# Optimization experiments

Measured on AMD Instinct MI355X. Metric: run time of the kernel, lower is better.

The kernel has to match this reference:

```python
import jax, jax.numpy as jnp
import numpy as np

N1, N2, N3, N4, D = 50000, 100000, 200000, 300000, 256


def setup_inputs() -> dict:
    key = jax.random.key(0)
    ks = jax.random.split(key, 10)
    feat = jax.random.normal(ks[0], (N1, D), dtype=jnp.float32) * 0.5  # scaled so level-4 products stay bounded
    c2a = jax.random.randint(ks[1], (N2,), 0, N1)
    c2b = jax.random.randint(ks[2], (N2,), 0, N1)
    c3a = jax.random.randint(ks[3], (N3,), 0, N2)
    c3b = jax.random.randint(ks[4], (N3,), 0, N2)
    c4a = jax.random.randint(ks[5], (N4,), 0, N3)
    c4b = jax.random.randint(ks[6], (N4,), 0, N3)
    W = jax.random.normal(ks[7], (D, D), dtype=jnp.float32) / jnp.sqrt(jnp.float32(D))
    b = jax.random.normal(ks[8], (D,), dtype=jnp.float32) * 0.01
    return {"feat": feat, "c2a": c2a, "c2b": c2b, "c3a": c3a, "c3b": c3b,
            "c4a": c4a, "c4b": c4b, "W": W, "b": b}


def _scatter_sum(h_parent, ca, cb, num_children):
    # each parent sends its feature to both children; children sum incoming messages
    z = jnp.zeros((num_children, h_parent.shape[1]), dtype=h_parent.dtype)
    return z.at[ca].add(h_parent).at[cb].add(h_parent)


def reference(feat, c2a, c2b, c3a, c3b, c4a, c4b, W, b):
    # upward: prod reduction over the two constituent subpaths (mailbox prod, dim=1)
    h1 = feat
    h2 = h1[c2a] * h1[c2b]            # [N2, D]
    h3 = h2[c3a] * h2[c3b]            # [N3, D]
    h4 = h3[c4a] * h3[c4b]            # [N4, D]
    # downward: sum-scatter parent -> children, h = h + h_down
    h3 = h3 + _scatter_sum(h4, c4a, c4b, h3.shape[0])
    h2 = h2 + _scatter_sum(h3, c3a, c3b, h2.shape[0])
    h1 = h1 + _scatter_sum(h2, c2a, c2b, h1.shape[0])
    # apply_nodes on n1: Linear + SiLU
    out = jax.nn.silu(h1 @ W + b)
    return out
```

## Files before the change

kernel.cpp:

```cpp
#include <hip/hip_runtime.h>
#include <cstdint>
#include <cstddef>

#define DD 256
#define DH 128
#define SCAN_BLK 256
#define SCAN_ELEMS 2048

__device__ __forceinline__ float2 mul2(float2 a, float2 b) {
    return make_float2(a.x * b.x, a.y * b.y);
}
__device__ __forceinline__ float2 add2(float2 a, float2 b) {
    return make_float2(a.x + b.x, a.y + b.y);
}
__device__ __forceinline__ float2 ldh(const float* __restrict__ base, int row, int lane) {
    return ((const float2*)(base + (size_t)row * DH))[lane];
}
__device__ __forceinline__ float2 ldf(const float* __restrict__ base, int row, int doff, int lane) {
    return ((const float2*)(base + (size_t)row * DD + doff))[lane];
}

__global__ void k_count_pairs(const int* __restrict__ ea, const int* __restrict__ eb,
                              int ne, int* __restrict__ cnt) {
    int e = blockIdx.x * blockDim.x + threadIdx.x;
    if (e >= ne) return;
    atomicAdd(&cnt[ea[e]], 1);
    atomicAdd(&cnt[eb[e]], 1);
}

__global__ void k_fill_edges(const int* __restrict__ ea, const int* __restrict__ eb,
                             int ne, int* __restrict__ cursor, int* __restrict__ ent) {
    int e = blockIdx.x * blockDim.x + threadIdx.x;
    if (e >= ne) return;
    int a = ea[e], b = eb[e];
    int pa = atomicAdd(&cursor[a], 1);
    int pb = atomicAdd(&cursor[b], 1);
    ent[pa] = e;
    ent[pb] = e;
}

__global__ void k_fill_pairs4(const int* __restrict__ c4a, const int* __restrict__ c4b,
                              const int* __restrict__ c3a, const int* __restrict__ c3b,
                              int ne, int* __restrict__ cursor, int2* __restrict__ entp) {
    int e = blockIdx.x * blockDim.x + threadIdx.x;
    if (e >= ne) return;
    int a = c4a[e], b = c4b[e];
    int2 prA = make_int2(c3a[b], c3b[b]);
    int2 prB = make_int2(c3a[a], c3b[a]);
    int pa = atomicAdd(&cursor[a], 1);
    int pb = atomicAdd(&cursor[b], 1);
    entp[pa] = prA;
    entp[pb] = prB;
}

__global__ void k_block_sums(const int* __restrict__ cnt, int n, int* __restrict__ bsum) {
    __shared__ int sdata[SCAN_BLK];
    int base = blockIdx.x * SCAN_ELEMS;
    int s = 0;
#pragma unroll
    for (int k = 0; k < 8; ++k) {
        int idx = base + threadIdx.x + k * SCAN_BLK;
        if (idx < n) s += cnt[idx];
    }
    sdata[threadIdx.x] = s;
    __syncthreads();
    for (int off = SCAN_BLK / 2; off > 0; off >>= 1) {
        if (threadIdx.x < off) sdata[threadIdx.x] += sdata[threadIdx.x + off];
        __syncthreads();
    }
    if (threadIdx.x == 0) bsum[blockIdx.x] = sdata[0];
}

__global__ void k_scan_bsums(int* __restrict__ bsum, int nb, int* __restrict__ total_out) {
    if (threadIdx.x == 0 && blockIdx.x == 0) {
        int acc = 0;
        for (int b = 0; b < nb; ++b) { int v = bsum[b]; bsum[b] = acc; acc += v; }
        *total_out = acc;
    }
}

__global__ void k_scan_final(const int* __restrict__ cnt, int n,
                             const int* __restrict__ bsum, int* __restrict__ offs) {
    __shared__ int sdata[SCAN_BLK];
    int base = blockIdx.x * SCAN_ELEMS;
    int t0 = base + threadIdx.x * 8;
    int loc[8];
    int s = 0;
#pragma unroll
    for (int k = 0; k < 8; ++k) {
        int idx = t0 + k;
        int v = (idx < n) ? cnt[idx] : 0;
        loc[k] = s;
        s += v;
    }
    sdata[threadIdx.x] = s;
    __syncthreads();
    int run = s;
    for (int off = 1; off < SCAN_BLK; off <<= 1) {
        int add = (threadIdx.x >= (unsigned)off) ? sdata[threadIdx.x - off] : 0;
        __syncthreads();
        run += add;
        sdata[threadIdx.x] = run;
        __syncthreads();
    }
    int texcl = run - s + bsum[blockIdx.x];
#pragma unroll
    for (int k = 0; k < 8; ++k) {
        int idx = t0 + k;
        if (idx < n) offs[idx] = texcl + loc[k];
    }
}

__global__ void k_h2_half(const float* __restrict__ feat, const int* __restrict__ c2a,
                          const int* __restrict__ c2b, float* __restrict__ h2h,
                          int n2, int doff) {
    int q = blockIdx.x * 4 + (threadIdx.x >> 6);
    int lane = threadIdx.x & 63;
    if (q >= n2) return;
    float2 v = mul2(ldf(feat, c2a[q], doff, lane), ldf(feat, c2b[q], doff, lane));
    ((float2*)(h2h + (size_t)q * DH))[lane] = v;
}

__global__ void k_h3tot_half(const float* __restrict__ h2h,
                             const int* __restrict__ c3a, const int* __restrict__ c3b,
                             const int* __restrict__ offs4, const int2* __restrict__ entp,
                             float* __restrict__ h3th, int lo, int hi) {
    int j = lo + blockIdx.x * 4 + (threadIdx.x >> 6);
    int lane = threadIdx.x & 63;
    if (j >= hi) return;
    float2 own = mul2(ldh(h2h, c3a[j], lane), ldh(h2h, c3b[j], lane));
    float2 s = make_float2(0.f, 0.f);
    int e0 = offs4[j], e1 = offs4[j + 1];
    int e = e0;
    for (; e + 1 < e1; e += 2) {
        int2 p0 = entp[e], p1 = entp[e + 1];
        float2 a0 = ldh(h2h, p0.x, lane), b0 = ldh(h2h, p0.y, lane);
        float2 a1 = ldh(h2h, p1.x, lane), b1 = ldh(h2h, p1.y, lane);
        s = add2(s, add2(mul2(a0, b0), mul2(a1, b1)));
    }
    if (e < e1) {
        int2 p = entp[e];
        s = add2(s, mul2(ldh(h2h, p.x, lane), ldh(h2h, p.y, lane)));
    }
    float2 r = mul2(own, make_float2(1.f + s.x, 1.f + s.y));
    ((float2*)(h3th + (size_t)(j - lo) * DH))[lane] = r;
}

__global__ void k_m2_half(const float* __restrict__ h2h,
                          const int* __restrict__ offs3, const int* __restrict__ ent3,
                          const float* __restrict__ h3th, float* __restrict__ dst,
                          int n2, int lo, int hi, int first) {
    int q = blockIdx.x * 4 + (threadIdx.x >> 6);
    int lane = threadIdx.x & 63;
    if (q >= n2) return;
    float2 h = first ? ldh(h2h, q, lane) : ldh(dst, q, lane);
    int f0 = offs3[q], f1 = offs3[q + 1];
    int f = f0;
    for (; f + 1 < f1; f += 2) {
        int j0 = ent3[f], j1 = ent3[f + 1];
        bool in0 = (j0 >= lo) && (j0 < hi);
        bool in1 = (j1 >= lo) && (j1 < hi);
        if (in0 && in1) {
            h = add2(h, add2(ldh(h3th, j0 - lo, lane), ldh(h3th, j1 - lo, lane)));
        } else if (in0) {
            h = add2(h, ldh(h3th, j0 - lo, lane));
        } else if (in1) {
            h = add2(h, ldh(h3th, j1 - lo, lane));
        }
    }
    if (f < f1) {
        int j0 = ent3[f];
        if (j0 >= lo && j0 < hi) h = add2(h, ldh(h3th, j0 - lo, lane));
    }
    ((float2*)(dst + (size_t)q * DH))[lane] = h;
}

__global__ void k_h1_half(const float* __restrict__ feat, const float* __restrict__ m2,
                          const int* __restrict__ offs2, const int* __restrict__ ent2,
                          float* __restrict__ out, int n1, int doff) {
    int i = blockIdx.x * 4 + (threadIdx.x >> 6);
    int lane = threadIdx.x & 63;
    if (i >= n1) return;
    float2 h = ldf(feat, i, doff, lane);
    int e0 = offs2[i], e1 = offs2[i + 1];
    int e = e0;
    for (; e + 1 < e1; e += 2) {
        int q0 = ent2[e], q1 = ent2[e + 1];
        h = add2(h, add2(ldh(m2, q0, lane), ldh(m2, q1, lane)));
    }
    if (e < e1) h = add2(h, ldh(m2, ent2[e], lane));
    ((float2*)(out + (size_t)i * DD + doff))[lane] = h;
}

__device__ __forceinline__ float silu_f(float x) { return x / (1.0f + expf(-x)); }

__global__ __launch_bounds__(256) void k_gemm_silu(float* __restrict__ h,
                                                   const float* __restrict__ W,
                                                   const float* __restrict__ bias,
                                                   int n1) {
    __shared__ float As[32 * DD];
    const int t = threadIdx.x;
    const int row0 = blockIdx.x * 32;

    const float4* hv = (const float4*)h;
    float4* As4 = (float4*)As;
#pragma unroll
    for (int i = 0; i < 8; ++i) {
        int idx = t + i * 256;
        int r = idx >> 6, c = idx & 63;
        int gr = row0 + r;
        float4 v = make_float4(0.f, 0.f, 0.f, 0.f);
        if (gr < n1) v = hv[(size_t)gr * 64 + c];
        As4[idx] = v;
    }
    __syncthreads();

    const int rg = t >> 6;
    const int cg = t & 63;
    const float4* Wv = (const float4*)W;

    float4 acc[8];
#pragma unroll
    for (int r = 0; r < 8; ++r) acc[r] = make_float4(0.f, 0.f, 0.f, 0.f);

    for (int k = 0; k < DD; k += 4) {
        float4 a[8];
#pragma unroll
        for (int r = 0; r < 8; ++r)
            a[r] = *(const float4*)&As[(rg * 8 + r) * DD + k];
#pragma unroll
        for (int kk = 0; kk < 4; ++kk) {
            float4 w = Wv[(size_t)(k + kk) * 64 + cg];
#pragma unroll
            for (int r = 0; r < 8; ++r) {
                float av = (kk == 0) ? a[r].x : (kk == 1) ? a[r].y
                         : (kk == 2) ? a[r].z : a[r].w;
                acc[r].x += av * w.x;
                acc[r].y += av * w.y;
                acc[r].z += av * w.z;
                acc[r].w += av * w.w;
            }
        }
    }

    float4 bb = ((const float4*)bias)[cg];
    float4* ho = (float4*)h;
#pragma unroll
    for (int r = 0; r < 8; ++r) {
        int gr = row0 + rg * 8 + r;
        if (gr >= n1) continue;
        float4 x = acc[r];
        x.x = silu_f(x.x + bb.x);
        x.y = silu_f(x.y + bb.y);
        x.z = silu_f(x.z + bb.z);
        x.w = silu_f(x.w + bb.w);
        ho[(size_t)gr * 64 + cg] = x;
    }
}

static inline size_t al16(size_t x) { return (x + 15) & ~(size_t)15; }

extern "C" void kernel_launch(void* const* d_in, const int* in_sizes, int n_in,
                              void* d_out, int out_size, void* d_ws, size_t ws_size,
                              hipStream_t stream) {
    const float* feat = (const float*)d_in[0];
    const int* c2a = (const int*)d_in[1];
    const int* c2b = (const int*)d_in[2];
    const int* c3a = (const int*)d_in[3];
    const int* c3b = (const int*)d_in[4];
    const int* c4a = (const int*)d_in[5];
    const int* c4b = (const int*)d_in[6];
    const float* W = (const float*)d_in[7];
    const float* bias = (const float*)d_in[8];

    const int N1 = in_sizes[0] / DD;
    const int N2 = in_sizes[1];
    const int N3 = in_sizes[3];
    const int N4 = in_sizes[5];
    float* out = (float*)d_out;
    char* ws = (char*)d_ws;

    dim3 blk(256);
    auto rows_grid = [](int n) { return dim3((unsigned)((n + 3) / 4)); };
    auto thr_grid = [](int n) { return dim3((unsigned)((n + 255) / 256)); };

    int maxN = N1 > N2 ? N1 : N2;
    if (N3 > maxN) maxN = N3;

    size_t cnt_b   = al16((size_t)maxN * 4);
    size_t bsum_b  = al16(4096);
    size_t offs4_b = al16((size_t)(N3 + 1) * 4);
    size_t entp_b  = al16((size_t)2 * N4 * 8);
    size_t offs3_b = al16((size_t)(N2 + 1) * 4);
    size_t ent3_b  = al16((size_t)2 * N3 * 4);
    size_t offs2_b = al16((size_t)(N1 + 1) * 4);
    size_t ent2_b  = al16((size_t)2 * N2 * 4);
    size_t fixed_b = cnt_b + bsum_b + offs4_b + entp_b + offs3_b + ent3_b +
                     offs2_b + ent2_b;
    size_t h2h_b = (size_t)N2 * DH * sizeof(float);
    size_t h3th_full_b = (size_t)N3 * DH * sizeof(float);

    char* p = ws;
    int* cnt   = (int*)p; p += cnt_b;
    int* bsum  = (int*)p; p += bsum_b;
    int* offs4 = (int*)p; p += offs4_b;
    int2* entp = (int2*)p; p += entp_b;
    int* offs3 = (int*)p; p += offs3_b;
    int* ent3  = (int*)p; p += ent3_b;
    int* offs2 = (int*)p; p += offs2_b;
    int* ent2  = (int*)p; p += ent2_b;
    float* h2h = (float*)p; p += h2h_b;

    bool single = (ws_size >= fixed_b + h2h_b + h3th_full_b);

    auto scan_offs = [&](int* cn, int nnode, int* offs) {
        int nb = (nnode + SCAN_ELEMS - 1) / SCAN_ELEMS;
        k_block_sums<<<dim3((unsigned)nb), dim3(SCAN_BLK), 0, stream>>>(cn, nnode, bsum);
        k_scan_bsums<<<dim3(1), dim3(64), 0, stream>>>(bsum, nb, offs + nnode);
        k_scan_final<<<dim3((unsigned)nb), dim3(SCAN_BLK), 0, stream>>>(cn, nnode, bsum, offs);
    };

    hipMemsetAsync(cnt, 0, (size_t)N3 * 4, stream);
    k_count_pairs<<<thr_grid(N4), blk, 0, stream>>>(c4a, c4b, N4, cnt);
    scan_offs(cnt, N3, offs4);
    hipMemcpyAsync(cnt, offs4, (size_t)N3 * 4, hipMemcpyDeviceToDevice, stream);
    k_fill_pairs4<<<thr_grid(N4), blk, 0, stream>>>(c4a, c4b, c3a, c3b, N4, cnt, entp);

    hipMemsetAsync(cnt, 0, (size_t)N2 * 4, stream);
    k_count_pairs<<<thr_grid(N3), blk, 0, stream>>>(c3a, c3b, N3, cnt);
    scan_offs(cnt, N2, offs3);
    hipMemcpyAsync(cnt, offs3, (size_t)N2 * 4, hipMemcpyDeviceToDevice, stream);
    k_fill_edges<<<thr_grid(N3), blk, 0, stream>>>(c3a, c3b, N3, cnt, ent3);

    hipMemsetAsync(cnt, 0, (size_t)N1 * 4, stream);
    k_count_pairs<<<thr_grid(N2), blk, 0, stream>>>(c2a, c2b, N2, cnt);
    scan_offs(cnt, N1, offs2);
    hipMemcpyAsync(cnt, offs2, (size_t)N1 * 4, hipMemcpyDeviceToDevice, stream);
    k_fill_edges<<<thr_grid(N2), blk, 0, stream>>>(c2a, c2b, N2, cnt, ent2);

    if (single) {
        float* h3th = (float*)p;
        for (int doff = 0; doff < DD; doff += DH) {
            k_h2_half<<<rows_grid(N2), blk, 0, stream>>>(feat, c2a, c2b, h2h, N2, doff);
            k_h3tot_half<<<rows_grid(N3), blk, 0, stream>>>(h2h, c3a, c3b, offs4, entp,
                                                            h3th, 0, N3);
            k_m2_half<<<rows_grid(N2), blk, 0, stream>>>(h2h, offs3, ent3, h3th,
                                                         h2h, N2, 0, N3, 1);
            k_h1_half<<<rows_grid(N1), blk, 0, stream>>>(feat, h2h, offs2, ent2,
                                                         out, N1, doff);
        }
    } else {
        float* m2h = (float*)p;
        char* pc = p + h2h_b;
        float* h3th = (float*)pc;
        size_t free_b = (ws_size > fixed_b + 2 * h2h_b) ? ws_size - fixed_b - 2 * h2h_b : 0;
        int chunk_rows = (int)(free_b / ((size_t)DH * sizeof(float)));
        if (chunk_rows > N3) chunk_rows = N3;
        if (chunk_rows < 1) chunk_rows = 1;
        int C = (N3 + chunk_rows - 1) / chunk_rows;
        chunk_rows = (N3 + C - 1) / C;

        for (int doff = 0; doff < DD; doff += DH) {
            k_h2_half<<<rows_grid(N2), blk, 0, stream>>>(feat, c2a, c2b, h2h, N2, doff);
            int first = 1;
            for (int lo = 0; lo < N3; lo += chunk_rows) {
                int hi = lo + chunk_rows;
                if (hi > N3) hi = N3;
                k_h3tot_half<<<rows_grid(hi - lo), blk, 0, stream>>>(h2h, c3a, c3b,
                                                                     offs4, entp,
                                                                     h3th, lo, hi);
                k_m2_half<<<rows_grid(N2), blk, 0, stream>>>(h2h, offs3, ent3, h3th,
                                                             m2h, N2, lo, hi, first);
                first = 0;
            }
            k_h1_half<<<rows_grid(N1), blk, 0, stream>>>(feat, m2h, offs2, ent2,
                                                         out, N1, doff);
        }
    }

    k_gemm_silu<<<dim3((unsigned)((N1 + 31) / 32)), blk, 0, stream>>>(out, W, bias, N1);
}
```

Baseline: 776.7 us.

## Widen gather kernels to float4 rows and fuse CSR build across levels

The gather and scatter kernels now give each row 32 threads loading float4 instead of 64 threads loading float2, and each block covers 8 rows. This cuts load instructions per gathered row and lets each wave hold more independent row gathers in flight. The CSR build for all three levels is merged into one count kernel and one fill kernel, and the scan writes the cursor array directly, which removes the device-to-device copies and several launches. The cost is separate count and cursor buffers for each level, so the fixed workspace grows and the chunked path may be chosen more often.

```diff
diff --git a/kernel.cpp b/kernel.cpp
--- a/kernel.cpp
+++ b/kernel.cpp
@@ -7,50 +7,63 @@
 #define SCAN_BLK 256
 #define SCAN_ELEMS 2048
 
-__device__ __forceinline__ float2 mul2(float2 a, float2 b) {
-    return make_float2(a.x * b.x, a.y * b.y);
-}
-__device__ __forceinline__ float2 add2(float2 a, float2 b) {
-    return make_float2(a.x + b.x, a.y + b.y);
-}
-__device__ __forceinline__ float2 ldh(const float* __restrict__ base, int row, int lane) {
-    return ((const float2*)(base + (size_t)row * DH))[lane];
-}
-__device__ __forceinline__ float2 ldf(const float* __restrict__ base, int row, int doff, int lane) {
-    return ((const float2*)(base + (size_t)row * DD + doff))[lane];
-}
-
-__global__ void k_count_pairs(const int* __restrict__ ea, const int* __restrict__ eb,
-                              int ne, int* __restrict__ cnt) {
+__device__ __forceinline__ float4 f4mul(float4 a, float4 b) {
+    return make_float4(a.x * b.x, a.y * b.y, a.z * b.z, a.w * b.w);
+}
+__device__ __forceinline__ float4 f4add(float4 a, float4 b) {
+    return make_float4(a.x + b.x, a.y + b.y, a.z + b.z, a.w + b.w);
+}
+__device__ __forceinline__ float4 ldh4(const float* __restrict__ base, int row, int sl) {
+    return ((const float4*)(base + (size_t)row * DH))[sl];
+}
+__device__ __forceinline__ float4 ldf4(const float* __restrict__ base, int row, int doff, int sl) {
+    return ((const float4*)(base + (size_t)row * DD + doff))[sl];
+}
+
+__global__ void k_count_all(const int* __restrict__ c2a, const int* __restrict__ c2b,
+                            const int* __restrict__ c3a, const int* __restrict__ c3b,
+                            const int* __restrict__ c4a, const int* __restrict__ c4b,
+                            int n2, int n3, int n4,
+                            int* __restrict__ cnt4, int* __restrict__ cnt3,
+                            int* __restrict__ cnt2) {
     int e = blockIdx.x * blockDim.x + threadIdx.x;
-    if (e >= ne) return;
-    atomicAdd(&cnt[ea[e]], 1);
-    atomicAdd(&cnt[eb[e]], 1);
-}
-
-__global__ void k_fill_edges(const int* __restrict__ ea, const int* __restrict__ eb,
-                             int ne, int* __restrict__ cursor, int* __restrict__ ent) {
+    if (e < n4) { atomicAdd(&cnt4[c4a[e]], 1); atomicAdd(&cnt4[c4b[e]], 1); }
+    if (e < n3) { atomicAdd(&cnt3[c3a[e]], 1); atomicAdd(&cnt3[c3b[e]], 1); }
+    if (e < n2) { atomicAdd(&cnt2[c2a[e]], 1); atomicAdd(&cnt2[c2b[e]], 1); }
+}
+
+__global__ void k_fill_all(const int* __restrict__ c2a, const int* __restrict__ c2b,
+                           const int* __restrict__ c3a, const int* __restrict__ c3b,
+                           const int* __restrict__ c4a, const int* __restrict__ c4b,
+                           int n2, int n3, int n4,
+                           int* __restrict__ cur4, int* __restrict__ cur3,
+                           int* __restrict__ cur2,
+                           int2* __restrict__ entp, int* __restrict__ ent3,
+                           int* __restrict__ ent2) {
     int e = blockIdx.x * blockDim.x + threadIdx.x;
-    if (e >= ne) return;
-    int a = ea[e], b = eb[e];
-    int pa = atomicAdd(&cursor[a], 1);
-    int pb = atomicAdd(&cursor[b], 1);
-    ent[pa] = e;
-    ent[pb] = e;
-}
-
-__global__ void k_fill_pairs4(const int* __restrict__ c4a, const int* __restrict__ c4b,
-                              const int* __restrict__ c3a, const int* __restrict__ c3b,
-                              int ne, int* __restrict__ cursor, int2* __restrict__ entp) {
-    int e = blockIdx.x * blockDim.x + threadIdx.x;
-    if (e >= ne) return;
-    int a = c4a[e], b = c4b[e];
-    int2 prA = make_int2(c3a[b], c3b[b]);
-    int2 prB = make_int2(c3a[a], c3b[a]);
-    int pa = atomicAdd(&cursor[a], 1);
-    int pb = atomicAdd(&cursor[b], 1);
-    entp[pa] = prA;
-    entp[pb] = prB;
+    if (e < n4) {
+        int a = c4a[e], b = c4b[e];
+        int2 prA = make_int2(c3a[b], c3b[b]);
+        int2 prB = make_int2(c3a[a], c3b[a]);
+        int pa = atomicAdd(&cur4[a], 1);
+        int pb = atomicAdd(&cur4[b], 1);
+        entp[pa] = prA;
+        entp[pb] = prB;
+    }
+    if (e < n3) {
+        int a = c3a[e], b = c3b[e];
+        int pa = atomicAdd(&cur3[a], 1);
+        int pb = atomicAdd(&cur3[b], 1);
+        ent3[pa] = e;
+        ent3[pb] = e;
+    }
+    if (e < n2) {
+        int a = c2a[e], b = c2b[e];
+        int pa = atomicAdd(&cur2[a], 1);
+        int pb = atomicAdd(&cur2[b], 1);
+        ent2[pa] = e;
+        ent2[pb] = e;
+    }
 }
 
 __global__ void k_block_sums(const int* __restrict__ cnt, int n, int* __restrict__ bsum) {
@@ -80,7 +93,8 @@
 }
 
 __global__ void k_scan_final(const int* __restrict__ cnt, int n,
-                             const int* __restrict__ bsum, int* __restrict__ offs) {
+                             const int* __restrict__ bsum, int* __restrict__ offs,
+                             int* __restrict__ cursor) {
     __shared__ int sdata[SCAN_BLK];
     int base = blockIdx.x * SCAN_ELEMS;
     int t0 = base + threadIdx.x * 8;
@@ -107,53 +121,57 @@
 #pragma unroll
     for (int k = 0; k < 8; ++k) {
         int idx = t0 + k;
-        if (idx < n) offs[idx] = texcl + loc[k];
+        if (idx < n) {
+            int v = texcl + loc[k];
+            offs[idx] = v;
+            cursor[idx] = v;
+        }
     }
 }
 
 __global__ void k_h2_half(const float* __restrict__ feat, const int* __restrict__ c2a,
                           const int* __restrict__ c2b, float* __restrict__ h2h,
                           int n2, int doff) {
-    int q = blockIdx.x * 4 + (threadIdx.x >> 6);
-    int lane = threadIdx.x & 63;
+    int q = blockIdx.x * 8 + (threadIdx.x >> 5);
+    int sl = threadIdx.x & 31;
     if (q >= n2) return;
-    float2 v = mul2(ldf(feat, c2a[q], doff, lane), ldf(feat, c2b[q], doff, lane));
-    ((float2*)(h2h + (size_t)q * DH))[lane] = v;
+    float4 v = f4mul(ldf4(feat, c2a[q], doff, sl), ldf4(feat, c2b[q], doff, sl));
+    ((float4*)(h2h + (size_t)q * DH))[sl] = v;
 }
 
 __global__ void k_h3tot_half(const float* __restrict__ h2h,
                              const int* __restrict__ c3a, const int* __restrict__ c3b,
                              const int* __restrict__ offs4, const int2* __restrict__ entp,
                              float* __restrict__ h3th, int lo, int hi) {
-    int j = lo + blockIdx.x * 4 + (threadIdx.x >> 6);
-    int lane = threadIdx.x & 63;
+    int j = lo + blockIdx.x * 8 + (threadIdx.x >> 5);
+    int sl = threadIdx.x & 31;
     if (j >= hi) return;
-    float2 own = mul2(ldh(h2h, c3a[j], lane), ldh(h2h, c3b[j], lane));
-    float2 s = make_float2(0.f, 0.f);
+    float4 own = f4mul(ldh4(h2h, c3a[j], sl), ldh4(h2h, c3b[j], sl));
+    float4 s = make_float4(0.f, 0.f, 0.f, 0.f);
     int e0 = offs4[j], e1 = offs4[j + 1];
     int e = e0;
     for (; e + 1 < e1; e += 2) {
         int2 p0 = entp[e], p1 = entp[e + 1];
-        float2 a0 = ldh(h2h, p0.x, lane), b0 = ldh(h2h, p0.y, lane);
-        float2 a1 = ldh(h2h, p1.x, lane), b1 = ldh(h2h, p1.y, lane);
-        s = add2(s, add2(mul2(a0, b0), mul2(a1, b1)));
+        float4 a0 = ldh4(h2h, p0.x, sl), b0 = ldh4(h2h, p0.y, sl);
+        float4 a1 = ldh4(h2h, p1.x, sl), b1 = ldh4(h2h, p1.y, sl);
+        s = f4add(s, f4add(f4mul(a0, b0), f4mul(a1, b1)));
     }
     if (e < e1) {
         int2 p = entp[e];
-        s = add2(s, mul2(ldh(h2h, p.x, lane), ldh(h2h, p.y, lane)));
-    }
-    float2 r = mul2(own, make_float2(1.f + s.x, 1.f + s.y));
-    ((float2*)(h3th + (size_t)(j - lo) * DH))[lane] = r;
+        s = f4add(s, f4mul(ldh4(h2h, p.x, sl), ldh4(h2h, p.y, sl)));
+    }
+    float4 r = f4mul(own, make_float4(1.f + s.x, 1.f + s.y, 1.f + s.z, 1.f + s.w));
+    ((float4*)(h3th + (size_t)(j - lo) * DH))[sl] = r;
 }
 
 __global__ void k_m2_half(const float* __restrict__ h2h,
                           const int* __restrict__ offs3, const int* __restrict__ ent3,
                           const float* __restrict__ h3th, float* __restrict__ dst,
                           int n2, int lo, int hi, int first) {
-    int q = blockIdx.x * 4 + (threadIdx.x >> 6);
-    int lane = threadIdx.x & 63;
+    int q = blockIdx.x * 8 + (threadIdx.x >> 5);
+    int sl = threadIdx.x & 31;
     if (q >= n2) return;
-    float2 h = first ? ldh(h2h, q, lane) : ldh(dst, q, lane);
+    float4 h = first ? ldh4(h2h, q, sl) : ldh4(dst, q, sl);
     int f0 = offs3[q], f1 = offs3[q + 1];
     int f = f0;
     for (; f + 1 < f1; f += 2) {
@@ -161,35 +179,35 @@
         bool in0 = (j0 >= lo) && (j0 < hi);
         bool in1 = (j1 >= lo) && (j1 < hi);
         if (in0 && in1) {
-            h = add2(h, add2(ldh(h3th, j0 - lo, lane), ldh(h3th, j1 - lo, lane)));
+            h = f4add(h, f4add(ldh4(h3th, j0 - lo, sl), ldh4(h3th, j1 - lo, sl)));
         } else if (in0) {
-            h = add2(h, ldh(h3th, j0 - lo, lane));
+            h = f4add(h, ldh4(h3th, j0 - lo, sl));
         } else if (in1) {
-            h = add2(h, ldh(h3th, j1 - lo, lane));
+            h = f4add(h, ldh4(h3th, j1 - lo, sl));
         }
     }
     if (f < f1) {
         int j0 = ent3[f];
-        if (j0 >= lo && j0 < hi) h = add2(h, ldh(h3th, j0 - lo, lane));
-    }
-    ((float2*)(dst + (size_t)q * DH))[lane] = h;
+        if (j0 >= lo && j0 < hi) h = f4add(h, ldh4(h3th, j0 - lo, sl));
+    }
+    ((float4*)(dst + (size_t)q * DH))[sl] = h;
 }
 
 __global__ void k_h1_half(const float* __restrict__ feat, const float* __restrict__ m2,
                           const int* __restrict__ offs2, const int* __restrict__ ent2,
                           float* __restrict__ out, int n1, int doff) {
-    int i = blockIdx.x * 4 + (threadIdx.x >> 6);
-    int lane = threadIdx.x & 63;
+    int i = blockIdx.x * 8 + (threadIdx.x >> 5);
+    int sl = threadIdx.x & 31;
     if (i >= n1) return;
-    float2 h = ldf(feat, i, doff, lane);
+    float4 h = ldf4(feat, i, doff, sl);
     int e0 = offs2[i], e1 = offs2[i + 1];
     int e = e0;
     for (; e + 1 < e1; e += 2) {
         int q0 = ent2[e], q1 = ent2[e + 1];
-        h = add2(h, add2(ldh(m2, q0, lane), ldh(m2, q1, lane)));
-    }
-    if (e < e1) h = add2(h, ldh(m2, ent2[e], lane));
-    ((float2*)(out + (size_t)i * DD + doff))[lane] = h;
+        h = f4add(h, f4add(ldh4(m2, q0, sl), ldh4(m2, q1, sl)));
+    }
+    if (e < e1) h = f4add(h, ldh4(m2, ent2[e], sl));
+    ((float4*)(out + (size_t)i * DD + doff))[sl] = h;
 }
 
 __device__ __forceinline__ float silu_f(float x) { return x / (1.0f + expf(-x)); }
@@ -281,13 +299,15 @@
     char* ws = (char*)d_ws;
 
     dim3 blk(256);
-    auto rows_grid = [](int n) { return dim3((unsigned)((n + 3) / 4)); };
+    auto rows_grid8 = [](int n) { return dim3((unsigned)((n + 7) / 8)); };
     auto thr_grid = [](int n) { return dim3((unsigned)((n + 255) / 256)); };
 
-    int maxN = N1 > N2 ? N1 : N2;
-    if (N3 > maxN) maxN = N3;
-
-    size_t cnt_b   = al16((size_t)maxN * 4);
+    size_t cnt4_b  = al16((size_t)N3 * 4);
+    size_t cnt3_b  = al16((size_t)N2 * 4);
+    size_t cnt2_b  = al16((size_t)N1 * 4);
+    size_t cur4_b  = al16((size_t)N3 * 4);
+    size_t cur3_b  = al16((size_t)N2 * 4);
+    size_t cur2_b  = al16((size_t)N1 * 4);
     size_t bsum_b  = al16(4096);
     size_t offs4_b = al16((size_t)(N3 + 1) * 4);
     size_t entp_b  = al16((size_t)2 * N4 * 8);
@@ -295,13 +315,18 @@
     size_t ent3_b  = al16((size_t)2 * N3 * 4);
     size_t offs2_b = al16((size_t)(N1 + 1) * 4);
     size_t ent2_b  = al16((size_t)2 * N2 * 4);
-    size_t fixed_b = cnt_b + bsum_b + offs4_b + entp_b + offs3_b + ent3_b +
-                     offs2_b + ent2_b;
+    size_t fixed_b = cnt4_b + cnt3_b + cnt2_b + cur4_b + cur3_b + cur2_b + bsum_b +
+                     offs4_b + entp_b + offs3_b + ent3_b + offs2_b + ent2_b;
     size_t h2h_b = (size_t)N2 * DH * sizeof(float);
     size_t h3th_full_b = (size_t)N3 * DH * sizeof(float);
 
     char* p = ws;
-    int* cnt   = (int*)p; p += cnt_b;
+    int* cnt4  = (int*)p; p += cnt4_b;
+    int* cnt3  = (int*)p; p += cnt3_b;
+    int* cnt2  = (int*)p; p += cnt2_b;
+    int* cur4  = (int*)p; p += cur4_b;
+    int* cur3  = (int*)p; p += cur3_b;
+    int* cur2  = (int*)p; p += cur2_b;
     int* bsum  = (int*)p; p += bsum_b;
     int* offs4 = (int*)p; p += offs4_b;
     int2* entp = (int2*)p; p += entp_b;
@@ -313,41 +338,36 @@
 
     bool single = (ws_size >= fixed_b + h2h_b + h3th_full_b);
 
-    auto scan_offs = [&](int* cn, int nnode, int* offs) {
+    auto scan_offs = [&](int* cn, int nnode, int* offs, int* cursor) {
         int nb = (nnode + SCAN_ELEMS - 1) / SCAN_ELEMS;
         k_block_sums<<<dim3((unsigned)nb), dim3(SCAN_BLK), 0, stream>>>(cn, nnode, bsum);
         k_scan_bsums<<<dim3(1), dim3(64), 0, stream>>>(bsum, nb, offs + nnode);
-        k_scan_final<<<dim3((unsigned)nb), dim3(SCAN_BLK), 0, stream>>>(cn, nnode, bsum, offs);
+        k_scan_final<<<dim3((unsigned)nb), dim3(SCAN_BLK), 0, stream>>>(cn, nnode, bsum,
+                                                                        offs, cursor);
     };
 
-    hipMemsetAsync(cnt, 0, (size_t)N3 * 4, stream);
-    k_count_pairs<<<thr_grid(N4), blk, 0, stream>>>(c4a, c4b, N4, cnt);
-    scan_offs(cnt, N3, offs4);
-    hipMemcpyAsync(cnt, offs4, (size_t)N3 * 4, hipMemcpyDeviceToDevice, stream);
-    k_fill_pairs4<<<thr_grid(N4), blk, 0, stream>>>(c4a, c4b, c3a, c3b, N4, cnt, entp);
-
-    hipMemsetAsync(cnt, 0, (size_t)N2 * 4, stream);
-    k_count_pairs<<<thr_grid(N3), blk, 0, stream>>>(c3a, c3b, N3, cnt);
-    scan_offs(cnt, N2, offs3);
-    hipMemcpyAsync(cnt, offs3, (size_t)N2 * 4, hipMemcpyDeviceToDevice, stream);
-    k_fill_edges<<<thr_grid(N3), blk, 0, stream>>>(c3a, c3b, N3, cnt, ent3);
-
-    hipMemsetAsync(cnt, 0, (size_t)N1 * 4, stream);
-    k_count_pairs<<<thr_grid(N2), blk, 0, stream>>>(c2a, c2b, N2, cnt);
-    scan_offs(cnt, N1, offs2);
-    hipMemcpyAsync(cnt, offs2, (size_t)N1 * 4, hipMemcpyDeviceToDevice, stream);
-    k_fill_edges<<<thr_grid(N2), blk, 0, stream>>>(c2a, c2b, N2, cnt, ent2);
+    int maxE = N2 > N3 ? N2 : N3;
+    if (N4 > maxE) maxE = N4;
+    hipMemsetAsync(cnt4, 0, cnt4_b + cnt3_b + cnt2_b, stream);
+    k_count_all<<<thr_grid(maxE), blk, 0, stream>>>(c2a, c2b, c3a, c3b, c4a, c4b,
+                                                    N2, N3, N4, cnt4, cnt3, cnt2);
+    scan_offs(cnt4, N3, offs4, cur4);
+    scan_offs(cnt3, N2, offs3, cur3);
+    scan_offs(cnt2, N1, offs2, cur2);
+    k_fill_all<<<thr_grid(maxE), blk, 0, stream>>>(c2a, c2b, c3a, c3b, c4a, c4b,
+                                                   N2, N3, N4, cur4, cur3, cur2,
+                                                   entp, ent3, ent2);
 
     if (single) {
         float* h3th = (float*)p;
         for (int doff = 0; doff < DD; doff += DH) {
-            k_h2_half<<<rows_grid(N2), blk, 0, stream>>>(feat, c2a, c2b, h2h, N2, doff);
-            k_h3tot_half<<<rows_grid(N3), blk, 0, stream>>>(h2h, c3a, c3b, offs4, entp,
-                                                            h3th, 0, N3);
-            k_m2_half<<<rows_grid(N2), blk, 0, stream>>>(h2h, offs3, ent3, h3th,
-                                                         h2h, N2, 0, N3, 1);
-            k_h1_half<<<rows_grid(N1), blk, 0, stream>>>(feat, h2h, offs2, ent2,
-                                                         out, N1, doff);
+            k_h2_half<<<rows_grid8(N2), blk, 0, stream>>>(feat, c2a, c2b, h2h, N2, doff);
+            k_h3tot_half<<<rows_grid8(N3), blk, 0, stream>>>(h2h, c3a, c3b, offs4, entp,
+                                                             h3th, 0, N3);
+            k_m2_half<<<rows_grid8(N2), blk, 0, stream>>>(h2h, offs3, ent3, h3th,
+                                                          h2h, N2, 0, N3, 1);
+            k_h1_half<<<rows_grid8(N1), blk, 0, stream>>>(feat, h2h, offs2, ent2,
+                                                          out, N1, doff);
         }
     } else {
         float* m2h = (float*)p;
@@ -361,20 +381,20 @@
         chunk_rows = (N3 + C - 1) / C;
 
         for (int doff = 0; doff < DD; doff += DH) {
-            k_h2_half<<<rows_grid(N2), blk, 0, stream>>>(feat, c2a, c2b, h2h, N2, doff);
+            k_h2_half<<<rows_grid8(N2), blk, 0, stream>>>(feat, c2a, c2b, h2h, N2, doff);
             int first = 1;
             for (int lo = 0; lo < N3; lo += chunk_rows) {
                 int hi = lo + chunk_rows;
                 if (hi > N3) hi = N3;
-                k_h3tot_half<<<rows_grid(hi - lo), blk, 0, stream>>>(h2h, c3a, c3b,
-                                                                     offs4, entp,
-                                                                     h3th, lo, hi);
-                k_m2_half<<<rows_grid(N2), blk, 0, stream>>>(h2h, offs3, ent3, h3th,
-                                                             m2h, N2, lo, hi, first);
+                k_h3tot_half<<<rows_grid8(hi - lo), blk, 0, stream>>>(h2h, c3a, c3b,
+                                                                      offs4, entp,
+                                                                      h3th, lo, hi);
+                k_m2_half<<<rows_grid8(N2), blk, 0, stream>>>(h2h, offs3, ent3, h3th,
+                                                              m2h, N2, lo, hi, first);
                 first = 0;
             }
-            k_h1_half<<<rows_grid(N1), blk, 0, stream>>>(feat, m2h, offs2, ent2,
-                                                         out, N1, doff);
+            k_h1_half<<<rows_grid8(N1), blk, 0, stream>>>(feat, m2h, offs2, ent2,
+                                                          out, N1, doff);
         }
     }
 
```

Measured after the change: 777.6 us. No clear change (+0.1%).
